# Optimization experiments

Measured on AMD Instinct MI355X. Metric: run time of the kernel, lower is better.

The kernel has to match this reference:

```python
import jax, jax.numpy as jnp
import numpy as np
from jax import lax


def setup_inputs() -> dict:
    key = jax.random.key(0)
    k1, k2, k3 = jax.random.split(key, 3)
    B, inCh, H, Wd = 8, 64, 96, 96
    outCh, sub, kh, kw = 64, 16, 3, 3
    X = jax.random.normal(k1, (B, inCh, H, Wd), dtype=jnp.float32)
    # mimic torch Conv2d default init scale ~ 1/sqrt(fan_in)
    scale = 1.0 / np.sqrt(sub * kh * kw)
    W = jax.random.normal(k2, (outCh, sub, kh, kw), dtype=jnp.float32) * scale
    b = jax.random.normal(k3, (outCh,), dtype=jnp.float32) * scale
    return {"X": X, "W": W, "b": b}


def reference(X, W, b):
    # X: [B, inCh, H, Wd]; W: [outCh, sub, kh, kw]; b: [outCh]
    B, inCh, H, Wd = X.shape
    outCh, sub, kh, kw = W.shape
    desired = outCh + sub - 1
    reps = -(-desired // inCh)  # ceil
    # tile channels then keep first `desired` channels (matches X.repeat + slice)
    Xr = jnp.tile(X, (1, reps, 1, 1))[:, :desired]  # [B, desired, H, Wd]
    # sliding overlapping channel window: out channel o uses channels [o, o+sub)
    idx = jnp.arange(outCh)[:, None] + jnp.arange(sub)[None, :]  # [outCh, sub]
    Xw = Xr[:, idx]                         # [B, outCh, sub, H, Wd]
    Xw = Xw.reshape(B, outCh * sub, H, Wd)  # grouped-conv layout
    # grouped valid conv: group g (= out channel) contracts its own sub channels
    out = lax.conv_general_dilated(
        Xw, W, window_strides=(1, 1), padding="VALID",
        dimension_numbers=("NCHW", "OIHW", "NCHW"),
        feature_group_count=outCh,
    )  # [B, outCh, H-kh+1, Wd-kw+1]
    return out + b[None, :, None, None]
```

## Files before the change

### kernel.cpp

```cpp
#include <hip/hip_runtime.h>


typedef _Float16 f16;
typedef _Float16 f16x8 __attribute__((ext_vector_type(8)));
typedef float    f32x16 __attribute__((ext_vector_type(16)));

constexpr int IN_H = 96, IN_W = 96, OUT_H = 94, OUT_W = 94;
constexpr int NCH = 64, NOC = 64, NSUB = 16, BATCH = 8;
constexpr int TILE_Y = 4;
constexpr int SROWS  = TILE_Y + 2;
constexpr int SXP    = 36;
constexpr size_t A_BYTES   = 2ull * 27 * 64 * 16;
constexpr size_t WS_NEEDED = A_BYTES + 256;

__device__ __forceinline__ int imin(int a, int b) { return a < b ? a : b; }

__global__ void build_a_k(const float* __restrict__ W, f16* __restrict__ Ah)
{
    const int e = blockIdx.x * 256 + threadIdx.x;
    if (e >= 2 * 27 * 64) return;
    const int lane = e & 63;
    const int r    = e >> 6;
    const int j    = r % 3;
    const int khw  = (r / 3) % 9;
    const int oh   = r / 27;
    const int cs   = oh ? (j == 0 ? 0 : j + 1) : j;
    const int kh = khw / 3, kw = khw % 3;
    const int o  = oh * 32 + (lane & 31);
    const int cb = cs * 16 + (lane >> 5) * 8;
    f16 v[8];
#pragma unroll
    for (int jj = 0; jj < 8; ++jj) {
        const int c = cb + jj;
        const int s = (c - o) & 63;
        v[jj] = (s < NSUB) ? (f16)W[((o * NSUB + s) * 3 + kh) * 3 + kw] : (f16)0.f;
    }
    *reinterpret_cast<f16x8*>(Ah + (size_t)e * 8) = *reinterpret_cast<f16x8*>(v);
}

__global__ __launch_bounds__(512, 2)
void sconv_fused(const float* __restrict__ Xg, const f16* __restrict__ Ah,
                 const float* __restrict__ Bg, float* __restrict__ Og)
{
    __shared__ __attribute__((aligned(16))) unsigned char lds[SROWS * SXP * 128];

    const int tid  = threadIdx.x;
    const int wave = tid >> 6;
    const int lane = tid & 63;

    const int x0 = blockIdx.x * 32;
    const int y0 = blockIdx.y * TILE_Y;
    const int b  = blockIdx.z;

    const float* __restrict__ Xb = Xg + (size_t)b * NCH * IN_H * IN_W;

    {
        const int xh = tid & 31;
        const int u  = tid >> 5;
        const int cg = u & 7;
        const int rb = u >> 3;
#pragma unroll
        for (int rr = 0; rr < 3; ++rr) {
            const int row = rb * 3 + rr;
            const int gy  = imin(y0 + row, IN_H - 1);
#pragma unroll
            for (int ci = 0; ci < 8; ++ci) {
                const int c = cg * 8 + ci;
                const float* __restrict__ p = Xb + ((size_t)c * IN_H + gy) * IN_W;
                const float f = p[imin(x0 + xh, IN_W - 1)];
                *reinterpret_cast<f16*>(lds + (((row * SXP + xh) << 7) +
                    ((cg ^ (xh & 7)) << 4) + (ci << 1))) = (f16)f;
                if (xh < 4) {
                    const int x2 = 32 + xh;
                    const float f2 = p[imin(x0 + x2, IN_W - 1)];
                    *reinterpret_cast<f16*>(lds + (((row * SXP + x2) << 7) +
                        ((cg ^ (x2 & 7)) << 4) + (ci << 1))) = (f16)f2;
                }
            }
        }
    }
    __syncthreads();

    const int oh = wave & 1;
    const int yy = wave >> 1;
    const int y  = y0 + yy;
    if (y >= OUT_H) return;

    const int px = lane & 31;
    const int kg = lane >> 5;

    f16x8 A[9][3];
    {
        const f16* Ab = Ah + (size_t)oh * 27 * 64 * 8;
#pragma unroll
        for (int khw = 0; khw < 9; ++khw)
#pragma unroll
            for (int j = 0; j < 3; ++j)
                A[khw][j] = *reinterpret_cast<const f16x8*>(
                    Ab + (((size_t)khw * 3 + j) * 64 + lane) * 8);
    }
    int cog[3];
    cog[0] = 0; cog[1] = oh ? 4 : 2; cog[2] = oh ? 6 : 4;

    f32x16 acc;
#pragma unroll
    for (int r = 0; r < 16; ++r)
        acc[r] = Bg[oh * 32 + (r & 3) + 8 * (r >> 2) + 4 * kg];

#pragma unroll
    for (int kh = 0; kh < 3; ++kh) {
#pragma unroll
        for (int kw = 0; kw < 3; ++kw) {
            const int xloc = px + kw;
            const int base = ((yy + kh) * SXP + xloc) << 7;
            const int sx   = xloc & 7;
            f16x8 bf[3];
#pragma unroll
            for (int j = 0; j < 3; ++j)
                bf[j] = *reinterpret_cast<const f16x8*>(
                    lds + base + (((cog[j] + kg) ^ sx) << 4));
#pragma unroll
            for (int j = 0; j < 3; ++j)
                acc = __builtin_amdgcn_mfma_f32_32x32x16_f16(
                          A[kh * 3 + kw][j], bf[j], acc, 0, 0, 0);
        }
    }

    const int x = x0 + px;
    if (x < OUT_W) {
#pragma unroll
        for (int r = 0; r < 16; ++r) {
            const int o = oh * 32 + (r & 3) + 8 * (r >> 2) + 4 * kg;
            Og[(((size_t)b * NOC + o) * OUT_H + y) * OUT_W + x] = acc[r];
        }
    }
}

constexpr int TILE_Xf = 16, TILE_Yf = 4, ROWSf = TILE_Yf + 2, COLSf = 19;
__global__ __launch_bounds__(256, 4)
void sconv_kernel(const float* __restrict__ Xg, const float* __restrict__ Wg,
                  const float* __restrict__ Bg, float* __restrict__ Og)
{
    __shared__ float Xs[NCH][ROWSf][COLSf];
    const int tid = threadIdx.x, wave = tid >> 6, lane = tid & 63;
    const int x = lane & 15, y4 = lane >> 4;
    const int tx0 = blockIdx.x * TILE_Xf, ty0 = blockIdx.y * TILE_Yf, b = blockIdx.z;
    const float* __restrict__ Xb = Xg + (size_t)b * NCH * IN_H * IN_W;
    for (int e = tid; e < NCH * ROWSf * 9; e += 256) {
        const int c = e / (ROWSf * 9), rm = e - c * (ROWSf * 9), r = rm / 9, c2 = rm - r * 9;
        int gy = ty0 + r;      if (gy > IN_H - 1) gy = IN_H - 1;
        int gx = tx0 + 2 * c2; if (gx > IN_W - 2) gx = IN_W - 2;
        const float2 v = *reinterpret_cast<const float2*>(Xb + (c * IN_H + gy) * IN_W + gx);
        Xs[c][r][2 * c2] = v.x; Xs[c][r][2 * c2 + 1] = v.y;
    }
    __syncthreads();
    float acc[16];
#pragma unroll
    for (int i = 0; i < 16; ++i) acc[i] = 0.f;
    const int o_base = __builtin_amdgcn_readfirstlane(wave << 4);
    for (int dd = 0; dd < 31; ++dd) {
        const int c = (o_base + dd) & 63;
        float xv[3][3];
#pragma unroll
        for (int r = 0; r < 3; ++r)
#pragma unroll
            for (int kw = 0; kw < 3; ++kw) xv[r][kw] = Xs[c][y4 + r][x + kw];
#pragma unroll
        for (int jp = 0; jp < 16; ++jp)
            if ((unsigned)(dd - jp) < 16u) {
                const float* __restrict__ wp = Wg + (((o_base + jp) * NSUB) + (dd - jp)) * 9;
#pragma unroll
                for (int kh = 0; kh < 3; ++kh)
#pragma unroll
                    for (int kw = 0; kw < 3; ++kw)
                        acc[jp] = fmaf(wp[kh * 3 + kw], xv[kh][kw], acc[jp]);
            }
    }
    const int y = ty0 + y4, xo = tx0 + x;
    if (y < OUT_H && xo < OUT_W)
#pragma unroll
        for (int jp = 0; jp < 16; ++jp) {
            const int o = o_base + jp;
            Og[(((size_t)b * NOC + o) * OUT_H + y) * OUT_W + xo] = acc[jp] + Bg[o];
        }
}

extern "C" void kernel_launch(void* const* d_in, const int* in_sizes, int n_in,
                              void* d_out, int out_size, void* d_ws, size_t ws_size,
                              hipStream_t stream)
{
    const float* X = (const float*)d_in[0];
    const float* W = (const float*)d_in[1];
    const float* B = (const float*)d_in[2];
    float* O = (float*)d_out;

    if (ws_size < WS_NEEDED) {
        dim3 grid((OUT_W + TILE_Xf - 1) / TILE_Xf, (OUT_H + TILE_Yf - 1) / TILE_Yf, BATCH);
        sconv_kernel<<<grid, 256, 0, stream>>>(X, W, B, O);
        return;
    }

    f16* Ah = (f16*)d_ws;
    build_a_k<<<14, 256, 0, stream>>>(W, Ah);
    dim3 grid(3, (OUT_H + TILE_Y - 1) / TILE_Y, BATCH);
    sconv_fused<<<grid, 512, 0, stream>>>(X, Ah, B, O);
}
```

Baseline: 92.05 us.

## Shrink row tile to two, use float4 channel loads, hoist A-fragment loads

Halves the output row tile per block to 2 (256 threads, 4 rows staged in LDS) and raises the grid to 47 row blocks. Input staging now uses float4 vector loads along x, with each thread handling one channel-row, in place of scalar loads. The A-fragment weight loads are issued before the staging so they overlap it. The bias add moves to the store. Smaller tiles mean more halo rereads per output row, but give more blocks and better occupancy for 94 rows that divide evenly by 2.

```diff
diff --git a/kernel.cpp b/kernel.cpp
--- a/kernel.cpp
+++ b/kernel.cpp
@@ -7,13 +7,11 @@
 
 constexpr int IN_H = 96, IN_W = 96, OUT_H = 94, OUT_W = 94;
 constexpr int NCH = 64, NOC = 64, NSUB = 16, BATCH = 8;
-constexpr int TILE_Y = 4;
+constexpr int TILE_Y = 2;
 constexpr int SROWS  = TILE_Y + 2;
 constexpr int SXP    = 36;
 constexpr size_t A_BYTES   = 2ull * 27 * 64 * 16;
 constexpr size_t WS_NEEDED = A_BYTES + 256;
-
-__device__ __forceinline__ int imin(int a, int b) { return a < b ? a : b; }
 
 __global__ void build_a_k(const float* __restrict__ W, f16* __restrict__ Ah)
 {
@@ -38,7 +36,7 @@
     *reinterpret_cast<f16x8*>(Ah + (size_t)e * 8) = *reinterpret_cast<f16x8*>(v);
 }
 
-__global__ __launch_bounds__(512, 2)
+__global__ __launch_bounds__(256, 3)
 void sconv_fused(const float* __restrict__ Xg, const f16* __restrict__ Ah,
                  const float* __restrict__ Bg, float* __restrict__ Og)
 {
@@ -47,47 +45,14 @@
     const int tid  = threadIdx.x;
     const int wave = tid >> 6;
     const int lane = tid & 63;
+    const int oh   = wave & 1;
+    const int yy   = wave >> 1;
+    const int px   = lane & 31;
+    const int kg   = lane >> 5;
 
     const int x0 = blockIdx.x * 32;
     const int y0 = blockIdx.y * TILE_Y;
     const int b  = blockIdx.z;
-
-    const float* __restrict__ Xb = Xg + (size_t)b * NCH * IN_H * IN_W;
-
-    {
-        const int xh = tid & 31;
-        const int u  = tid >> 5;
-        const int cg = u & 7;
-        const int rb = u >> 3;
-#pragma unroll
-        for (int rr = 0; rr < 3; ++rr) {
-            const int row = rb * 3 + rr;
-            const int gy  = imin(y0 + row, IN_H - 1);
-#pragma unroll
-            for (int ci = 0; ci < 8; ++ci) {
-                const int c = cg * 8 + ci;
-                const float* __restrict__ p = Xb + ((size_t)c * IN_H + gy) * IN_W;
-                const float f = p[imin(x0 + xh, IN_W - 1)];
-                *reinterpret_cast<f16*>(lds + (((row * SXP + xh) << 7) +
-                    ((cg ^ (xh & 7)) << 4) + (ci << 1))) = (f16)f;
-                if (xh < 4) {
-                    const int x2 = 32 + xh;
-                    const float f2 = p[imin(x0 + x2, IN_W - 1)];
-                    *reinterpret_cast<f16*>(lds + (((row * SXP + x2) << 7) +
-                        ((cg ^ (x2 & 7)) << 4) + (ci << 1))) = (f16)f2;
-                }
-            }
-        }
-    }
-    __syncthreads();
-
-    const int oh = wave & 1;
-    const int yy = wave >> 1;
-    const int y  = y0 + yy;
-    if (y >= OUT_H) return;
-
-    const int px = lane & 31;
-    const int kg = lane >> 5;
 
     f16x8 A[9][3];
     {
@@ -99,13 +64,35 @@
                 A[khw][j] = *reinterpret_cast<const f16x8*>(
                     Ab + (((size_t)khw * 3 + j) * 64 + lane) * 8);
     }
+
+    {
+        const int c   = tid >> 2;
+        const int row = tid & 3;
+        const int g   = c >> 3, cl = c & 7;
+        const float* __restrict__ p =
+            Xg + (((size_t)b * NCH + c) * IN_H + (y0 + row)) * IN_W;
+#pragma unroll
+        for (int i = 0; i < 9; ++i) {
+            const int xs = 4 * i;
+            int gx = x0 + xs; if (gx > IN_W - 4) gx = IN_W - 4;
+            const float4 v = *reinterpret_cast<const float4*>(p + gx);
+            const float vv[4] = {v.x, v.y, v.z, v.w};
+#pragma unroll
+            for (int q = 0; q < 4; ++q) {
+                const int xl = xs + q;
+                *reinterpret_cast<f16*>(lds + (((row * SXP + xl) << 7) +
+                    ((g ^ (xl & 7)) << 4) + (cl << 1))) = (f16)vv[q];
+            }
+        }
+    }
+    __syncthreads();
+
     int cog[3];
     cog[0] = 0; cog[1] = oh ? 4 : 2; cog[2] = oh ? 6 : 4;
 
     f32x16 acc;
 #pragma unroll
-    for (int r = 0; r < 16; ++r)
-        acc[r] = Bg[oh * 32 + (r & 3) + 8 * (r >> 2) + 4 * kg];
+    for (int r = 0; r < 16; ++r) acc[r] = 0.f;
 
 #pragma unroll
     for (int kh = 0; kh < 3; ++kh) {
@@ -126,12 +113,13 @@
         }
     }
 
+    const int y = y0 + yy;
     const int x = x0 + px;
     if (x < OUT_W) {
 #pragma unroll
         for (int r = 0; r < 16; ++r) {
             const int o = oh * 32 + (r & 3) + 8 * (r >> 2) + 4 * kg;
-            Og[(((size_t)b * NOC + o) * OUT_H + y) * OUT_W + x] = acc[r];
+            Og[(((size_t)b * NOC + o) * OUT_H + y) * OUT_W + x] = acc[r] + Bg[o];
         }
     }
 }
@@ -202,6 +190,6 @@
 
     f16* Ah = (f16*)d_ws;
     build_a_k<<<14, 256, 0, stream>>>(W, Ah);
-    dim3 grid(3, (OUT_H + TILE_Y - 1) / TILE_Y, BATCH);
-    sconv_fused<<<grid, 512, 0, stream>>>(X, Ah, B, O);
+    dim3 grid(3, OUT_H / TILE_Y, BATCH);
+    sconv_fused<<<grid, 256, 0, stream>>>(X, Ah, B, O);
 }
```

New measurement: 92.00 us. No clear change (-0.1%).
